# Kernel tuning notes

Hardware: AMD Instinct MI355X
Metric: run time of the kernel (lower is better)

The kernel has to match this reference:

```python
import jax, jax.numpy as jnp
import numpy as np

B, S, H, F, E, K = 2, 2048, 1024, 2816, 8, 2

def setup_inputs() -> dict:
    key = jax.random.key(0)
    k0, k1, k2, k3, k4 = jax.random.split(key, 5)
    return {
        "hidden_states": jax.random.normal(k0, (B, S, H), dtype=jnp.float32),
        "router_w": jax.random.normal(k1, (E, H), dtype=jnp.float32) * (1.0 / np.sqrt(H)),
        "w_gate": jax.random.normal(k2, (E, H, F), dtype=jnp.float32) * (1.0 / np.sqrt(H)),
        "w_up": jax.random.normal(k3, (E, H, F), dtype=jnp.float32) * (1.0 / np.sqrt(H)),
        "w_down": jax.random.normal(k4, (E, F, H), dtype=jnp.float32) * (1.0 / np.sqrt(F)),
    }

def reference(hidden_states, router_w, w_gate, w_up, w_down):
    # Router: logits [B,S,E], top-k routing with softmax over the k selected logits.
    router_logits = jnp.einsum("bsh,eh->bse", hidden_states, router_w)
    topk_values, topk_indices = jax.lax.top_k(router_logits, K)  # [B,S,K]
    topk_weights = jax.nn.softmax(topk_values.astype(jnp.float32), axis=-1).astype(hidden_states.dtype)

    x = hidden_states.reshape(-1, H)            # [T,H], T = B*S
    flat_idx = topk_indices.reshape(-1, K)      # [T,K] (int)
    flat_w = topk_weights.reshape(-1, K)        # [T,K]

    mixed = jnp.zeros_like(x)
    for e in range(E):  # small fixed expert loop; tokens fully vectorized
        # per-token combine weight for expert e (0 if not routed here)
        w_e = jnp.sum(jnp.where(flat_idx == e, flat_w, jnp.zeros_like(flat_w)), axis=-1)[:, None]
        # SwiGLU expert MLP: down(silu(gate(x)) * up(x))
        y = (jax.nn.silu(x @ w_gate[e]) * (x @ w_up[e])) @ w_down[e]
        mixed = mixed + w_e * y
    mixed_output = mixed.reshape(hidden_states.shape)

    # Load-balancing aux loss (Switch-style)
    router_probs = jax.nn.softmax(router_logits.astype(jnp.float32), axis=-1)
    P = router_probs.mean(axis=(0, 1))                                   # [E]
    f = jax.nn.one_hot(topk_indices, E, dtype=jnp.float32).mean(axis=(0, 1, 2))  # [E]
    aux_loss = E * jnp.sum(f * P)
    return mixed_output, aux_loss
```

## Files before the change

### kernel.cpp

```cpp
#include <hip/hip_runtime.h>
#include <hip/hip_bf16.h>
#include <stdint.h>

#define T_TOK 4096
#define H_DIM 1024
#define F_DIM 2816
#define E_NUM 8
#define ROWS_CAP 9216
#define TOTAL_MT 72

typedef float  f32x4  __attribute__((ext_vector_type(4)));
typedef __bf16 bf16x8 __attribute__((ext_vector_type(8)));

__device__ __forceinline__ unsigned short f32_bf16(float f) {
  union { float f; unsigned u; } v; v.f = f;
  unsigned r = v.u + 0x7fffu + ((v.u >> 16) & 1u);
  return (unsigned short)(r >> 16);
}

__device__ __forceinline__ void async16(const void* g, void* l) {
  __builtin_amdgcn_global_load_lds(
      (__attribute__((address_space(1))) void*)(g),
      (__attribute__((address_space(3))) void*)(l),
      16, 0, 0);
}

__device__ __forceinline__ f32x4 mfma16(bf16x8 a, bf16x8 b, f32x4 c) {
  return __builtin_amdgcn_mfma_f32_16x16x32_bf16(a, b, c, 0, 0, 0);
}


__global__ __launch_bounds__(256) void conv_x_kernel(const float* __restrict__ x,
                                                     unsigned short* __restrict__ xb) {
  int i = blockIdx.x * 256 + threadIdx.x;
  float4 v = ((const float4*)x)[i];
  ushort4 o;
  o.x = f32_bf16(v.x); o.y = f32_bf16(v.y); o.z = f32_bf16(v.z); o.w = f32_bf16(v.w);
  ((ushort4*)xb)[i] = o;
}

__global__ __launch_bounds__(256) void transpose_all(const float* __restrict__ wg,
                                                     const float* __restrict__ wu,
                                                     const float* __restrict__ wd,
                                                     unsigned short* __restrict__ Wgt,
                                                     unsigned short* __restrict__ Wut,
                                                     unsigned short* __restrict__ Wdt) {
  int bx = blockIdx.x;
  int mz = bx / 704, local = bx % 704;
  const float* s; unsigned short* d; int R, C, tx;
  size_t mat = (size_t)H_DIM * F_DIM;
  if (mz == 0)      { s = wg; d = Wgt; R = H_DIM; C = F_DIM; tx = 44; }
  else if (mz == 1) { s = wu; d = Wut; R = H_DIM; C = F_DIM; tx = 44; }
  else              { s = wd; d = Wdt; R = F_DIM; C = H_DIM; tx = 16; }
  int c0 = (local % tx) * 64;
  int rg0 = (local / tx) * 64;
  int e = blockIdx.y;
  s += e * mat; d += e * mat;
  int r0 = rg0;

  __shared__ float tile[64 * 65];
  int tid = threadIdx.x;
  int rr = tid >> 4, c4 = tid & 15;
#pragma unroll
  for (int it = 0; it < 4; it++) {
    int r = rr + 16 * it;
    float4 v = *(const float4*)(s + (size_t)(r0 + r) * C + c0 + c4 * 4);
    tile[r * 65 + c4 * 4 + 0] = v.x;
    tile[r * 65 + c4 * 4 + 1] = v.y;
    tile[r * 65 + c4 * 4 + 2] = v.z;
    tile[r * 65 + c4 * 4 + 3] = v.w;
  }
  __syncthreads();
  int cc = tid >> 4, r4 = tid & 15;
#pragma unroll
  for (int it = 0; it < 4; it++) {
    int c = cc + 16 * it;
    ushort4 o;
    o.x = f32_bf16(tile[(r4 * 4 + 0) * 65 + c]);
    o.y = f32_bf16(tile[(r4 * 4 + 1) * 65 + c]);
    o.z = f32_bf16(tile[(r4 * 4 + 2) * 65 + c]);
    o.w = f32_bf16(tile[(r4 * 4 + 3) * 65 + c]);
    *(ushort4*)(d + (size_t)(c0 + c) * R + r0 + r4 * 4) = o;
  }
}


__global__ __launch_bounds__(256) void router_kernel(const float* __restrict__ x,
                                                     const float* __restrict__ rw,
                                                     int* __restrict__ t2i,
                                                     float* __restrict__ t2w,
                                                     int* __restrict__ counts,
                                                     float* __restrict__ psum) {
  __shared__ float srw[E_NUM * H_DIM];
  __shared__ float sP[E_NUM];
  __shared__ int sC[E_NUM];
  int tid = threadIdx.x;
  for (int i = tid; i < E_NUM * H_DIM; i += 256) srw[i] = rw[i];
  if (tid < E_NUM) { sP[tid] = 0.f; sC[tid] = 0; }
  __syncthreads();
  int w = tid >> 6, lane = tid & 63;
  for (int it = 0; it < 4; ++it) {
    int t = blockIdx.x * 16 + w * 4 + it;
    float acc[E_NUM];
#pragma unroll
    for (int e = 0; e < E_NUM; e++) acc[e] = 0.f;
    const float* xr = x + (size_t)t * H_DIM;
    for (int h = lane; h < H_DIM; h += 64) {
      float xv = xr[h];
#pragma unroll
      for (int e = 0; e < E_NUM; e++) acc[e] += xv * srw[e * H_DIM + h];
    }
#pragma unroll
    for (int e = 0; e < E_NUM; e++) {
      float v = acc[e];
      for (int o = 32; o > 0; o >>= 1) v += __shfl_down(v, o, 64);
      acc[e] = __shfl(v, 0, 64);
    }
    if (lane == 0) {
      float mx = acc[0];
#pragma unroll
      for (int e = 1; e < E_NUM; e++) mx = fmaxf(mx, acc[e]);
      float pr[E_NUM], s = 0.f;
#pragma unroll
      for (int e = 0; e < E_NUM; e++) { pr[e] = __expf(acc[e] - mx); s += pr[e]; }
      float inv = 1.f / s;
#pragma unroll
      for (int e = 0; e < E_NUM; e++) atomicAdd(&sP[e], pr[e] * inv);
      int i0 = 0; float v0 = acc[0];
#pragma unroll
      for (int e = 1; e < E_NUM; e++) if (acc[e] > v0) { v0 = acc[e]; i0 = e; }
      int i1 = -1; float v1 = -3.4e38f;
#pragma unroll
      for (int e = 0; e < E_NUM; e++) if (e != i0 && acc[e] > v1) { v1 = acc[e]; i1 = e; }
      float e1 = __expf(v1 - v0);
      float w0 = 1.f / (1.f + e1);
      t2i[2 * t] = i0; t2i[2 * t + 1] = i1;
      t2w[2 * t] = w0; t2w[2 * t + 1] = e1 * w0;
      atomicAdd(&sC[i0], 1); atomicAdd(&sC[i1], 1);
    }
  }
  __syncthreads();
  if (tid < E_NUM) { atomicAdd(&counts[tid], sC[tid]); atomicAdd(&psum[tid], sP[tid]); }
}

__global__ void scan_aux_kernel(const int* __restrict__ counts, const float* __restrict__ psum,
                                int* __restrict__ offsets, int* __restrict__ cursors,
                                float* __restrict__ aux_out) {
  if (threadIdx.x == 0 && blockIdx.x == 0) {
    int off = 0; float aux = 0.f;
    for (int e = 0; e < E_NUM; e++) {
      offsets[e] = off;
      cursors[e] = off;
      off += (counts[e] + 127) & ~127;
      aux += ((float)counts[e] / 8192.0f) * (psum[e] / 4096.0f);
    }
    offsets[E_NUM] = off;
    *aux_out = 8.0f * aux;
  }
}

__global__ __launch_bounds__(256) void assign_kernel(const int* __restrict__ t2i,
                                                     const float* __restrict__ t2w,
                                                     int* __restrict__ cursors,
                                                     int* __restrict__ row2token,
                                                     float* __restrict__ roww,
                                                     int* __restrict__ t2row) {
  int t = blockIdx.x * 256 + threadIdx.x;
#pragma unroll
  for (int s = 0; s < 2; s++) {
    int e = t2i[2 * t + s];
    int p = atomicAdd(&cursors[e], 1);
    row2token[p] = t;
    roww[p] = t2w[2 * t + s];
    t2row[2 * t + s] = p;
  }
}

__device__ __forceinline__ int find_expert(const int* __restrict__ offsets, int row0,
                                           int& off_out) {
  int esel = -1, off = 0;
#pragma unroll
  for (int e = 0; e < E_NUM; e++) {
    int lo = offsets[e], hi = offsets[e + 1];
    if (row0 >= lo && row0 < hi) { esel = e; off = lo; }
  }
  off_out = off;
  return esel;
}

__global__ __launch_bounds__(256) void gateup_kernel(
    const unsigned short* __restrict__ xb,
    const unsigned short* __restrict__ wgt,
    const unsigned short* __restrict__ wut,
    unsigned short* __restrict__ act,
    const int* __restrict__ counts, const int* __restrict__ offsets,
    const int* __restrict__ row2token) {
  int g = blockIdx.x;
  int row0 = g * 128;
  int off;
  int e = find_expert(offsets, row0, off);
  if (e < 0) return;
  int cnt = counts[e];
  int rowbase = row0 - off;
  int ntile = blockIdx.y;

  __shared__ __align__(16) unsigned short smA[128 * 32];
  __shared__ __align__(16) unsigned short smG[64 * 32];
  __shared__ __align__(16) unsigned short smU[64 * 32];

  int tid = threadIdx.x;
  int w = tid >> 6, lane = tid & 63;
  int wm = w & 1, wn = w >> 1;

  int cA0 = w * 64 + lane;
  int rA0 = cA0 >> 2, qA0 = cA0 & 3;
  int rA1 = rA0 + 64;
  int tok0 = (rowbase + rA0 < cnt) ? row2token[off + rowbase + rA0] : 0;
  int tok1 = (rowbase + rA1 < cnt) ? row2token[off + rowbase + rA1] : 0;
  const unsigned short* gA0 = xb + (size_t)tok0 * H_DIM + qA0 * 8;
  const unsigned short* gA1 = xb + (size_t)tok1 * H_DIM + qA0 * 8;
  size_t wb = (size_t)e * F_DIM * H_DIM;
  const unsigned short* gG = wgt + wb + (size_t)(ntile * 64 + rA0) * H_DIM + qA0 * 8;
  const unsigned short* gU = wut + wb + (size_t)(ntile * 64 + rA0) * H_DIM + qA0 * 8;
  unsigned short* lA0 = smA + (w * 64) * 8;
  unsigned short* lA1 = smA + (256 + w * 64) * 8;
  unsigned short* lG = smG + (w * 64) * 8;
  unsigned short* lU = smU + (w * 64) * 8;

  f32x4 accg[4][2], accu[4][2];
#pragma unroll
  for (int i = 0; i < 4; i++)
#pragma unroll
    for (int j = 0; j < 2; j++) {
      accg[i][j] = (f32x4){0.f, 0.f, 0.f, 0.f};
      accu[i][j] = (f32x4){0.f, 0.f, 0.f, 0.f};
    }

  int m = lane & 15, quad = lane >> 4;
  for (int k0 = 0; k0 < H_DIM; k0 += 32) {
    async16(gA0 + k0, lA0);
    async16(gA1 + k0, lA1);
    async16(gG + k0, lG);
    async16(gU + k0, lU);
    __syncthreads();
    bf16x8 a[4], bg[2], bu[2];
#pragma unroll
    for (int i = 0; i < 4; i++)
      a[i] = *(const bf16x8*)(smA + (wm * 64 + 16 * i + m) * 32 + quad * 8);
#pragma unroll
    for (int j = 0; j < 2; j++) {
      bg[j] = *(const bf16x8*)(smG + (wn * 32 + 16 * j + m) * 32 + quad * 8);
      bu[j] = *(const bf16x8*)(smU + (wn * 32 + 16 * j + m) * 32 + quad * 8);
    }
#pragma unroll
    for (int i = 0; i < 4; i++)
#pragma unroll
      for (int j = 0; j < 2; j++) {
        accg[i][j] = mfma16(a[i], bg[j], accg[i][j]);
        accu[i][j] = mfma16(a[i], bu[j], accu[i][j]);
      }
    __syncthreads();
  }

#pragma unroll
  for (int i = 0; i < 4; i++)
#pragma unroll
    for (int j = 0; j < 2; j++)
#pragma unroll
      for (int r = 0; r < 4; r++) {
        int rt = wm * 64 + 16 * i + quad * 4 + r;
        int ct = wn * 32 + 16 * j + m;
        float g2 = accg[i][j][r], u = accu[i][j][r];
        float sv = g2 / (1.f + __expf(-g2)) * u;
        act[(size_t)(off + rowbase + rt) * F_DIM + ntile * 64 + ct] = f32_bf16(sv);
      }
}

__global__ __launch_bounds__(256) void down_kernel(
    const unsigned short* __restrict__ act,
    const unsigned short* __restrict__ wdt,
    const int* __restrict__ counts, const int* __restrict__ offsets,
    const float* __restrict__ roww,
    float* __restrict__ Y) {
  int g = blockIdx.x;
  int row0 = g * 128;
  int off;
  int e = find_expert(offsets, row0, off);
  if (e < 0) return;
  int cnt = counts[e];
  int rowbase = row0 - off;
  int ntile = blockIdx.y;
  int ks = blockIdx.z;
  int kbase = ks * (F_DIM / 2);

  __shared__ __align__(16) unsigned short smA[128 * 32];
  __shared__ __align__(16) unsigned short smB[128 * 32];

  int tid = threadIdx.x;
  int w = tid >> 6, lane = tid & 63;
  int wm = w & 1, wn = w >> 1;

  int r0 = tid >> 2, q0 = tid & 3;
  int r1 = r0 + 64;
  const unsigned short* gA0 = act + (size_t)(off + rowbase + r0) * F_DIM + kbase + q0 * 8;
  const unsigned short* gA1 = act + (size_t)(off + rowbase + r1) * F_DIM + kbase + q0 * 8;
  size_t wb = (size_t)e * H_DIM * F_DIM;
  const unsigned short* gB0 = wdt + wb + (size_t)(ntile * 128 + r0) * F_DIM + kbase + q0 * 8;
  const unsigned short* gB1 = wdt + wb + (size_t)(ntile * 128 + r1) * F_DIM + kbase + q0 * 8;
  unsigned short* lA0 = smA + tid * 8;
  unsigned short* lA1 = smA + (tid + 256) * 8;
  unsigned short* lB0 = smB + tid * 8;
  unsigned short* lB1 = smB + (tid + 256) * 8;

  f32x4 acc[4][4];
#pragma unroll
  for (int i = 0; i < 4; i++)
#pragma unroll
    for (int j = 0; j < 4; j++) acc[i][j] = (f32x4){0.f, 0.f, 0.f, 0.f};

  int m = lane & 15, quad = lane >> 4;
  for (int k0 = 0; k0 < F_DIM / 2; k0 += 32) {
    async16(gA0 + k0, lA0);
    async16(gA1 + k0, lA1);
    async16(gB0 + k0, lB0);
    async16(gB1 + k0, lB1);
    __syncthreads();
    bf16x8 a[4], b[4];
#pragma unroll
    for (int i = 0; i < 4; i++) {
      a[i] = *(const bf16x8*)(smA + (wm * 64 + 16 * i + m) * 32 + quad * 8);
      b[i] = *(const bf16x8*)(smB + (wn * 64 + 16 * i + m) * 32 + quad * 8);
    }
#pragma unroll
    for (int i = 0; i < 4; i++)
#pragma unroll
      for (int j = 0; j < 4; j++) acc[i][j] = mfma16(a[i], b[j], acc[i][j]);
    __syncthreads();
  }

  float* Yk = Y + (size_t)ks * ROWS_CAP * H_DIM;
#pragma unroll
  for (int i = 0; i < 4; i++)
#pragma unroll
    for (int r = 0; r < 4; r++) {
      int rt = wm * 64 + 16 * i + quad * 4 + r;
      int lrow = rowbase + rt;
      if (lrow < cnt) {
        float cw = roww[off + lrow];
#pragma unroll
        for (int j = 0; j < 4; j++) {
          int h = ntile * 128 + wn * 64 + 16 * j + m;
          Yk[(size_t)(off + lrow) * H_DIM + h] = cw * acc[i][j][r];
        }
      }
    }
}

__global__ __launch_bounds__(256) void combine_kernel(const float* __restrict__ Y,
                                                      const int* __restrict__ t2row,
                                                      float* __restrict__ out) {
  int t = blockIdx.x, hc = threadIdx.x;
  int r0 = t2row[2 * t], r1 = t2row[2 * t + 1];
  const float* Y1 = Y + (size_t)ROWS_CAP * H_DIM;
  float4 a = ((const float4*)(Y  + (size_t)r0 * H_DIM))[hc];
  float4 b = ((const float4*)(Y  + (size_t)r1 * H_DIM))[hc];
  float4 c = ((const float4*)(Y1 + (size_t)r0 * H_DIM))[hc];
  float4 d = ((const float4*)(Y1 + (size_t)r1 * H_DIM))[hc];
  float4 o;
  o.x = (a.x + b.x) + (c.x + d.x);
  o.y = (a.y + b.y) + (c.y + d.y);
  o.z = (a.z + b.z) + (c.z + d.z);
  o.w = (a.w + b.w) + (c.w + d.w);
  ((float4*)(out + (size_t)t * H_DIM))[hc] = o;
}


extern "C" void kernel_launch(void* const* d_in, const int* in_sizes, int n_in,
                              void* d_out, int out_size, void* d_ws, size_t ws_size,
                              hipStream_t stream) {
  const float* x  = (const float*)d_in[0];
  const float* rw = (const float*)d_in[1];
  const float* wg = (const float*)d_in[2];
  const float* wu = (const float*)d_in[3];
  const float* wd = (const float*)d_in[4];
  float* out = (float*)d_out;

  char* ws = (char*)d_ws;
  size_t p = 0;
  auto alloc = [&](size_t bytes) {
    char* r = ws + p;
    p = (p + bytes + 255) & ~(size_t)255;
    return r;
  };
  unsigned short* Xb  = (unsigned short*)alloc((size_t)T_TOK * H_DIM * 2);
  unsigned short* Wgt = (unsigned short*)alloc((size_t)E_NUM * F_DIM * H_DIM * 2);
  unsigned short* Wut = (unsigned short*)alloc((size_t)E_NUM * F_DIM * H_DIM * 2);
  unsigned short* Wdt = (unsigned short*)alloc((size_t)E_NUM * H_DIM * F_DIM * 2);
  unsigned short* Act = (unsigned short*)alloc((size_t)ROWS_CAP * F_DIM * 2);
  int*   t2i = (int*)alloc(T_TOK * 2 * 4);
  float* t2w = (float*)alloc(T_TOK * 2 * 4);
  int*   t2row = (int*)alloc(T_TOK * 2 * 4);
  int*   row2token = (int*)alloc(ROWS_CAP * 4);
  float* roww = (float*)alloc(ROWS_CAP * 4);
  int* ctrs = (int*)alloc(64 * 4);
  int* counts  = ctrs;
  int* cursors = ctrs + 8;
  float* psum  = (float*)(ctrs + 16);
  int* offsets = ctrs + 24;
  float* Y = (float*)Wgt;

  hipMemsetAsync(ctrs, 0, 96, stream);

  conv_x_kernel<<<T_TOK * H_DIM / 4 / 256, 256, 0, stream>>>(x, Xb);
  transpose_all<<<dim3(2112, E_NUM), 256, 0, stream>>>(wg, wu, wd, Wgt, Wut, Wdt);

  router_kernel<<<T_TOK / 16, 256, 0, stream>>>(x, rw, t2i, t2w, counts, psum);
  scan_aux_kernel<<<1, 64, 0, stream>>>(counts, psum, offsets, cursors, out + (size_t)T_TOK * H_DIM);
  assign_kernel<<<T_TOK / 256, 256, 0, stream>>>(t2i, t2w, cursors, row2token, roww, t2row);

  gateup_kernel<<<dim3(TOTAL_MT, F_DIM / 64), 256, 0, stream>>>(Xb, Wgt, Wut, Act, counts, offsets, row2token);
  down_kernel<<<dim3(TOTAL_MT, H_DIM / 128, 2), 256, 0, stream>>>(Act, Wdt, counts, offsets, roww, Y);
  combine_kernel<<<T_TOK, 256, 0, stream>>>(Y, t2row, out);
}
```

Measured before the change: 627.6 us.

## Double-buffer LDS tiles with async prefetch and XOR swizzle in expert GEMMs

Both the gate/up and down GEMM kernels now keep two LDS buffers and issue the global-to-LDS async loads for the next K step before computing on the current one. Explicit vmcnt waits and raw barriers replace __syncthreads, so load latency can overlap with MFMA work. The column chunk index is also XOR-swizzled by row on both the global source and the LDS read side, which is meant to reduce LDS bank conflicts. The cost is double the shared memory per block, which may lower occupancy, and correctness now depends on the hand-written waitcnt counts.

```diff
diff --git a/kernel.cpp b/kernel.cpp
--- a/kernel.cpp
+++ b/kernel.cpp
@@ -204,28 +204,28 @@
   int rowbase = row0 - off;
   int ntile = blockIdx.y;
 
-  __shared__ __align__(16) unsigned short smA[128 * 32];
-  __shared__ __align__(16) unsigned short smG[64 * 32];
-  __shared__ __align__(16) unsigned short smU[64 * 32];
+  __shared__ __align__(16) unsigned short smA[2][128 * 32];
+  __shared__ __align__(16) unsigned short smG[2][64 * 32];
+  __shared__ __align__(16) unsigned short smU[2][64 * 32];
 
   int tid = threadIdx.x;
   int w = tid >> 6, lane = tid & 63;
   int wm = w & 1, wn = w >> 1;
 
-  int cA0 = w * 64 + lane;
-  int rA0 = cA0 >> 2, qA0 = cA0 & 3;
+  int rA0 = tid >> 2, qA0 = tid & 3;
+  int qs = qA0 ^ ((rA0 >> 1) & 3);
   int rA1 = rA0 + 64;
   int tok0 = (rowbase + rA0 < cnt) ? row2token[off + rowbase + rA0] : 0;
   int tok1 = (rowbase + rA1 < cnt) ? row2token[off + rowbase + rA1] : 0;
-  const unsigned short* gA0 = xb + (size_t)tok0 * H_DIM + qA0 * 8;
-  const unsigned short* gA1 = xb + (size_t)tok1 * H_DIM + qA0 * 8;
+  const unsigned short* gA0 = xb + (size_t)tok0 * H_DIM + qs * 8;
+  const unsigned short* gA1 = xb + (size_t)tok1 * H_DIM + qs * 8;
   size_t wb = (size_t)e * F_DIM * H_DIM;
-  const unsigned short* gG = wgt + wb + (size_t)(ntile * 64 + rA0) * H_DIM + qA0 * 8;
-  const unsigned short* gU = wut + wb + (size_t)(ntile * 64 + rA0) * H_DIM + qA0 * 8;
-  unsigned short* lA0 = smA + (w * 64) * 8;
-  unsigned short* lA1 = smA + (256 + w * 64) * 8;
-  unsigned short* lG = smG + (w * 64) * 8;
-  unsigned short* lU = smU + (w * 64) * 8;
+  const unsigned short* gG = wgt + wb + (size_t)(ntile * 64 + rA0) * H_DIM + qs * 8;
+  const unsigned short* gU = wut + wb + (size_t)(ntile * 64 + rA0) * H_DIM + qs * 8;
+  unsigned short* lA0 = &smA[0][0] + (w * 64) * 8;
+  unsigned short* lA1 = &smA[0][0] + (256 + w * 64) * 8;
+  unsigned short* lG = &smG[0][0] + (w * 64) * 8;
+  unsigned short* lU = &smU[0][0] + (w * 64) * 8;
 
   f32x4 accg[4][2], accu[4][2];
 #pragma unroll
@@ -237,20 +237,37 @@
     }
 
   int m = lane & 15, quad = lane >> 4;
-  for (int k0 = 0; k0 < H_DIM; k0 += 32) {
-    async16(gA0 + k0, lA0);
-    async16(gA1 + k0, lA1);
-    async16(gG + k0, lG);
-    async16(gU + k0, lU);
-    __syncthreads();
+  int co = (quad ^ ((m >> 1) & 3)) * 8;
+
+#define GU_STAGE(buf, k0)                                \
+  do {                                                   \
+    async16(gA0 + (k0), lA0 + (buf) * (128 * 32));       \
+    async16(gA1 + (k0), lA1 + (buf) * (128 * 32));       \
+    async16(gG + (k0), lG + (buf) * (64 * 32));          \
+    async16(gU + (k0), lU + (buf) * (64 * 32));          \
+  } while (0)
+
+  GU_STAGE(0, 0);
+  int cur = 0;
+  for (int t = 0; t < 32; ++t) {
+    if (t < 31) {
+      GU_STAGE(cur ^ 1, (t + 1) * 32);
+      asm volatile("s_waitcnt vmcnt(4)" ::: "memory");
+    } else {
+      asm volatile("s_waitcnt vmcnt(0)" ::: "memory");
+    }
+    __builtin_amdgcn_s_barrier();
+    const unsigned short* bA = smA[cur];
+    const unsigned short* bG = smG[cur];
+    const unsigned short* bU = smU[cur];
     bf16x8 a[4], bg[2], bu[2];
 #pragma unroll
     for (int i = 0; i < 4; i++)
-      a[i] = *(const bf16x8*)(smA + (wm * 64 + 16 * i + m) * 32 + quad * 8);
+      a[i] = *(const bf16x8*)(bA + (wm * 64 + 16 * i + m) * 32 + co);
 #pragma unroll
     for (int j = 0; j < 2; j++) {
-      bg[j] = *(const bf16x8*)(smG + (wn * 32 + 16 * j + m) * 32 + quad * 8);
-      bu[j] = *(const bf16x8*)(smU + (wn * 32 + 16 * j + m) * 32 + quad * 8);
+      bg[j] = *(const bf16x8*)(bG + (wn * 32 + 16 * j + m) * 32 + co);
+      bu[j] = *(const bf16x8*)(bU + (wn * 32 + 16 * j + m) * 32 + co);
     }
 #pragma unroll
     for (int i = 0; i < 4; i++)
@@ -259,8 +276,10 @@
         accg[i][j] = mfma16(a[i], bg[j], accg[i][j]);
         accu[i][j] = mfma16(a[i], bu[j], accu[i][j]);
       }
-    __syncthreads();
-  }
+    __builtin_amdgcn_s_barrier();
+    cur ^= 1;
+  }
+#undef GU_STAGE
 
 #pragma unroll
   for (int i = 0; i < 4; i++)
@@ -293,24 +312,25 @@
   int ks = blockIdx.z;
   int kbase = ks * (F_DIM / 2);
 
-  __shared__ __align__(16) unsigned short smA[128 * 32];
-  __shared__ __align__(16) unsigned short smB[128 * 32];
+  __shared__ __align__(16) unsigned short smA[2][128 * 32];
+  __shared__ __align__(16) unsigned short smB[2][128 * 32];
 
   int tid = threadIdx.x;
   int w = tid >> 6, lane = tid & 63;
   int wm = w & 1, wn = w >> 1;
 
   int r0 = tid >> 2, q0 = tid & 3;
+  int qs = q0 ^ ((r0 >> 1) & 3);
   int r1 = r0 + 64;
-  const unsigned short* gA0 = act + (size_t)(off + rowbase + r0) * F_DIM + kbase + q0 * 8;
-  const unsigned short* gA1 = act + (size_t)(off + rowbase + r1) * F_DIM + kbase + q0 * 8;
+  const unsigned short* gA0 = act + (size_t)(off + rowbase + r0) * F_DIM + kbase + qs * 8;
+  const unsigned short* gA1 = act + (size_t)(off + rowbase + r1) * F_DIM + kbase + qs * 8;
   size_t wb = (size_t)e * H_DIM * F_DIM;
-  const unsigned short* gB0 = wdt + wb + (size_t)(ntile * 128 + r0) * F_DIM + kbase + q0 * 8;
-  const unsigned short* gB1 = wdt + wb + (size_t)(ntile * 128 + r1) * F_DIM + kbase + q0 * 8;
-  unsigned short* lA0 = smA + tid * 8;
-  unsigned short* lA1 = smA + (tid + 256) * 8;
-  unsigned short* lB0 = smB + tid * 8;
-  unsigned short* lB1 = smB + (tid + 256) * 8;
+  const unsigned short* gB0 = wdt + wb + (size_t)(ntile * 128 + r0) * F_DIM + kbase + qs * 8;
+  const unsigned short* gB1 = wdt + wb + (size_t)(ntile * 128 + r1) * F_DIM + kbase + qs * 8;
+  unsigned short* lA0 = &smA[0][0] + tid * 8;
+  unsigned short* lA1 = &smA[0][0] + (tid + 256) * 8;
+  unsigned short* lB0 = &smB[0][0] + tid * 8;
+  unsigned short* lB1 = &smB[0][0] + (tid + 256) * 8;
 
   f32x4 acc[4][4];
 #pragma unroll
@@ -319,24 +339,42 @@
     for (int j = 0; j < 4; j++) acc[i][j] = (f32x4){0.f, 0.f, 0.f, 0.f};
 
   int m = lane & 15, quad = lane >> 4;
-  for (int k0 = 0; k0 < F_DIM / 2; k0 += 32) {
-    async16(gA0 + k0, lA0);
-    async16(gA1 + k0, lA1);
-    async16(gB0 + k0, lB0);
-    async16(gB1 + k0, lB1);
-    __syncthreads();
+  int co = (quad ^ ((m >> 1) & 3)) * 8;
+
+#define DN_STAGE(buf, k0)                                \
+  do {                                                   \
+    async16(gA0 + (k0), lA0 + (buf) * (128 * 32));       \
+    async16(gA1 + (k0), lA1 + (buf) * (128 * 32));       \
+    async16(gB0 + (k0), lB0 + (buf) * (128 * 32));       \
+    async16(gB1 + (k0), lB1 + (buf) * (128 * 32));       \
+  } while (0)
+
+  DN_STAGE(0, 0);
+  int cur = 0;
+  for (int t = 0; t < 44; ++t) {
+    if (t < 43) {
+      DN_STAGE(cur ^ 1, (t + 1) * 32);
+      asm volatile("s_waitcnt vmcnt(4)" ::: "memory");
+    } else {
+      asm volatile("s_waitcnt vmcnt(0)" ::: "memory");
+    }
+    __builtin_amdgcn_s_barrier();
+    const unsigned short* bA = smA[cur];
+    const unsigned short* bB = smB[cur];
     bf16x8 a[4], b[4];
 #pragma unroll
     for (int i = 0; i < 4; i++) {
-      a[i] = *(const bf16x8*)(smA + (wm * 64 + 16 * i + m) * 32 + quad * 8);
-      b[i] = *(const bf16x8*)(smB + (wn * 64 + 16 * i + m) * 32 + quad * 8);
+      a[i] = *(const bf16x8*)(bA + (wm * 64 + 16 * i + m) * 32 + co);
+      b[i] = *(const bf16x8*)(bB + (wn * 64 + 16 * i + m) * 32 + co);
     }
 #pragma unroll
     for (int i = 0; i < 4; i++)
 #pragma unroll
       for (int j = 0; j < 4; j++) acc[i][j] = mfma16(a[i], b[j], acc[i][j]);
-    __syncthreads();
-  }
+    __builtin_amdgcn_s_barrier();
+    cur ^= 1;
+  }
+#undef DN_STAGE
 
   float* Yk = Y + (size_t)ks * ROWS_CAP * H_DIM;
 #pragma unroll
```

After: 639.6 us. Within noise of the previous version (+1.9%).

## Fuse x conversion into router, swizzle LDS layout, remap block order

Applied to the files above, without the earlier changes.

Removes the separate fp32-to-bf16 conversion kernel by doing the conversion inside the router kernel. It also applies an XOR swizzle to the 16-byte chunk positions used by the global-to-LDS copies and the MFMA operand reads, aiming to reduce LDS bank conflicts. Finally, it remaps the block index in the gate/up and down kernels so that consecutive blocks land on different row tiles, intended to spread weight reads across XCDs and improve L2 reuse. The remapping adds integer index arithmetic at the start of each block, and the swizzle must stay consistent between the writes and the reads.

```diff
diff --git a/kernel.cpp b/kernel.cpp
--- a/kernel.cpp
+++ b/kernel.cpp
@@ -27,16 +27,6 @@
 
 __device__ __forceinline__ f32x4 mfma16(bf16x8 a, bf16x8 b, f32x4 c) {
   return __builtin_amdgcn_mfma_f32_16x16x32_bf16(a, b, c, 0, 0, 0);
-}
-
-
-__global__ __launch_bounds__(256) void conv_x_kernel(const float* __restrict__ x,
-                                                     unsigned short* __restrict__ xb) {
-  int i = blockIdx.x * 256 + threadIdx.x;
-  float4 v = ((const float4*)x)[i];
-  ushort4 o;
-  o.x = f32_bf16(v.x); o.y = f32_bf16(v.y); o.z = f32_bf16(v.z); o.w = f32_bf16(v.w);
-  ((ushort4*)xb)[i] = o;
 }
 
 __global__ __launch_bounds__(256) void transpose_all(const float* __restrict__ wg,
@@ -87,6 +77,7 @@
 
 __global__ __launch_bounds__(256) void router_kernel(const float* __restrict__ x,
                                                      const float* __restrict__ rw,
+                                                     unsigned short* __restrict__ xb,
                                                      int* __restrict__ t2i,
                                                      float* __restrict__ t2w,
                                                      int* __restrict__ counts,
@@ -97,6 +88,19 @@
   int tid = threadIdx.x;
   for (int i = tid; i < E_NUM * H_DIM; i += 256) srw[i] = rw[i];
   if (tid < E_NUM) { sP[tid] = 0.f; sC[tid] = 0; }
+  {
+    size_t base = (size_t)blockIdx.x * 16 * H_DIM;
+    const float4* src = (const float4*)(x + base);
+    ushort4* dst = (ushort4*)(xb + base);
+#pragma unroll
+    for (int it = 0; it < 16; it++) {
+      int i = tid + it * 256;
+      float4 v = src[i];
+      ushort4 o;
+      o.x = f32_bf16(v.x); o.y = f32_bf16(v.y); o.z = f32_bf16(v.z); o.w = f32_bf16(v.w);
+      dst[i] = o;
+    }
+  }
   __syncthreads();
   int w = tid >> 6, lane = tid & 63;
   for (int it = 0; it < 4; ++it) {
@@ -195,14 +199,17 @@
     unsigned short* __restrict__ act,
     const int* __restrict__ counts, const int* __restrict__ offsets,
     const int* __restrict__ row2token) {
-  int g = blockIdx.x;
+  int L = blockIdx.y * 72 + blockIdx.x;
+  int c8 = L & 7, pos = L >> 3;
+  int ntile = pos / 9;
+  int g = c8 * 9 + pos % 9;
+
   int row0 = g * 128;
   int off;
   int e = find_expert(offsets, row0, off);
   if (e < 0) return;
   int cnt = counts[e];
   int rowbase = row0 - off;
-  int ntile = blockIdx.y;
 
   __shared__ __align__(16) unsigned short smA[128 * 32];
   __shared__ __align__(16) unsigned short smG[64 * 32];
@@ -212,16 +219,16 @@
   int w = tid >> 6, lane = tid & 63;
   int wm = w & 1, wn = w >> 1;
 
-  int cA0 = w * 64 + lane;
-  int rA0 = cA0 >> 2, qA0 = cA0 & 3;
+  int rA0 = tid >> 2, qA0 = tid & 3;
+  int qs = qA0 ^ ((rA0 >> 1) & 3);
   int rA1 = rA0 + 64;
   int tok0 = (rowbase + rA0 < cnt) ? row2token[off + rowbase + rA0] : 0;
   int tok1 = (rowbase + rA1 < cnt) ? row2token[off + rowbase + rA1] : 0;
-  const unsigned short* gA0 = xb + (size_t)tok0 * H_DIM + qA0 * 8;
-  const unsigned short* gA1 = xb + (size_t)tok1 * H_DIM + qA0 * 8;
+  const unsigned short* gA0 = xb + (size_t)tok0 * H_DIM + qs * 8;
+  const unsigned short* gA1 = xb + (size_t)tok1 * H_DIM + qs * 8;
   size_t wb = (size_t)e * F_DIM * H_DIM;
-  const unsigned short* gG = wgt + wb + (size_t)(ntile * 64 + rA0) * H_DIM + qA0 * 8;
-  const unsigned short* gU = wut + wb + (size_t)(ntile * 64 + rA0) * H_DIM + qA0 * 8;
+  const unsigned short* gG = wgt + wb + (size_t)(ntile * 64 + rA0) * H_DIM + qs * 8;
+  const unsigned short* gU = wut + wb + (size_t)(ntile * 64 + rA0) * H_DIM + qs * 8;
   unsigned short* lA0 = smA + (w * 64) * 8;
   unsigned short* lA1 = smA + (256 + w * 64) * 8;
   unsigned short* lG = smG + (w * 64) * 8;
@@ -237,6 +244,8 @@
     }
 
   int m = lane & 15, quad = lane >> 4;
+  int co = (quad ^ ((m >> 1) & 3)) * 8;
+
   for (int k0 = 0; k0 < H_DIM; k0 += 32) {
     async16(gA0 + k0, lA0);
     async16(gA1 + k0, lA1);
@@ -246,11 +255,11 @@
     bf16x8 a[4], bg[2], bu[2];
 #pragma unroll
     for (int i = 0; i < 4; i++)
-      a[i] = *(const bf16x8*)(smA + (wm * 64 + 16 * i + m) * 32 + quad * 8);
+      a[i] = *(const bf16x8*)(smA + (wm * 64 + 16 * i + m) * 32 + co);
 #pragma unroll
     for (int j = 0; j < 2; j++) {
-      bg[j] = *(const bf16x8*)(smG + (wn * 32 + 16 * j + m) * 32 + quad * 8);
-      bu[j] = *(const bf16x8*)(smU + (wn * 32 + 16 * j + m) * 32 + quad * 8);
+      bg[j] = *(const bf16x8*)(smG + (wn * 32 + 16 * j + m) * 32 + co);
+      bu[j] = *(const bf16x8*)(smU + (wn * 32 + 16 * j + m) * 32 + co);
     }
 #pragma unroll
     for (int i = 0; i < 4; i++)
@@ -282,15 +291,19 @@
     const int* __restrict__ counts, const int* __restrict__ offsets,
     const float* __restrict__ roww,
     float* __restrict__ Y) {
-  int g = blockIdx.x;
+  int L = (blockIdx.z * 8 + blockIdx.y) * 72 + blockIdx.x;
+  int c8 = L & 7, pos = L >> 3;
+  int g = c8 * 9 + pos % 9;
+  int rest = pos / 9;
+  int ntile = rest & 7;
+  int ks = rest >> 3;
+
   int row0 = g * 128;
   int off;
   int e = find_expert(offsets, row0, off);
   if (e < 0) return;
   int cnt = counts[e];
   int rowbase = row0 - off;
-  int ntile = blockIdx.y;
-  int ks = blockIdx.z;
   int kbase = ks * (F_DIM / 2);
 
   __shared__ __align__(16) unsigned short smA[128 * 32];
@@ -301,12 +314,13 @@
   int wm = w & 1, wn = w >> 1;
 
   int r0 = tid >> 2, q0 = tid & 3;
+  int qs = q0 ^ ((r0 >> 1) & 3);
   int r1 = r0 + 64;
-  const unsigned short* gA0 = act + (size_t)(off + rowbase + r0) * F_DIM + kbase + q0 * 8;
-  const unsigned short* gA1 = act + (size_t)(off + rowbase + r1) * F_DIM + kbase + q0 * 8;
+  const unsigned short* gA0 = act + (size_t)(off + rowbase + r0) * F_DIM + kbase + qs * 8;
+  const unsigned short* gA1 = act + (size_t)(off + rowbase + r1) * F_DIM + kbase + qs * 8;
   size_t wb = (size_t)e * H_DIM * F_DIM;
-  const unsigned short* gB0 = wdt + wb + (size_t)(ntile * 128 + r0) * F_DIM + kbase + q0 * 8;
-  const unsigned short* gB1 = wdt + wb + (size_t)(ntile * 128 + r1) * F_DIM + kbase + q0 * 8;
+  const unsigned short* gB0 = wdt + wb + (size_t)(ntile * 128 + r0) * F_DIM + kbase + qs * 8;
+  const unsigned short* gB1 = wdt + wb + (size_t)(ntile * 128 + r1) * F_DIM + kbase + qs * 8;
   unsigned short* lA0 = smA + tid * 8;
   unsigned short* lA1 = smA + (tid + 256) * 8;
   unsigned short* lB0 = smB + tid * 8;
@@ -319,6 +333,8 @@
     for (int j = 0; j < 4; j++) acc[i][j] = (f32x4){0.f, 0.f, 0.f, 0.f};
 
   int m = lane & 15, quad = lane >> 4;
+  int co = (quad ^ ((m >> 1) & 3)) * 8;
+
   for (int k0 = 0; k0 < F_DIM / 2; k0 += 32) {
     async16(gA0 + k0, lA0);
     async16(gA1 + k0, lA1);
@@ -328,8 +344,8 @@
     bf16x8 a[4], b[4];
 #pragma unroll
     for (int i = 0; i < 4; i++) {
-      a[i] = *(const bf16x8*)(smA + (wm * 64 + 16 * i + m) * 32 + quad * 8);
-      b[i] = *(const bf16x8*)(smB + (wn * 64 + 16 * i + m) * 32 + quad * 8);
+      a[i] = *(const bf16x8*)(smA + (wm * 64 + 16 * i + m) * 32 + co);
+      b[i] = *(const bf16x8*)(smB + (wn * 64 + 16 * i + m) * 32 + co);
     }
 #pragma unroll
     for (int i = 0; i < 4; i++)
@@ -411,10 +427,9 @@
 
   hipMemsetAsync(ctrs, 0, 96, stream);
 
-  conv_x_kernel<<<T_TOK * H_DIM / 4 / 256, 256, 0, stream>>>(x, Xb);
   transpose_all<<<dim3(2112, E_NUM), 256, 0, stream>>>(wg, wu, wd, Wgt, Wut, Wdt);
 
-  router_kernel<<<T_TOK / 16, 256, 0, stream>>>(x, rw, t2i, t2w, counts, psum);
+  router_kernel<<<T_TOK / 16, 256, 0, stream>>>(x, rw, Xb, t2i, t2w, counts, psum);
   scan_aux_kernel<<<1, 64, 0, stream>>>(counts, psum, offsets, cursors, out + (size_t)T_TOK * H_DIM);
   assign_kernel<<<T_TOK / 256, 256, 0, stream>>>(t2i, t2w, cursors, row2token, roww, t2row);
 
```

Result: faster. 609.5 us (-2.9%).
